# Kernel optimization log

Measured on AMD Instinct MI355X. Metric: run time of the kernel, lower is better.

Reference implementation:

```python
import jax, jax.numpy as jnp
import numpy as np

B, D, L = 32768, 1024, 4

def setup_inputs() -> dict:
    key = jax.random.key(0)
    k1, k2, k3 = jax.random.split(key, 3)
    x = jax.random.normal(k1, (B, D), dtype=jnp.float32)
    # torch init: normal_(0, 0.005) for both weights and biases, shape (d,1) -> flatten to (d,)
    weights = jax.random.normal(k2, (L, D), dtype=jnp.float32) * 0.005
    biases = jax.random.normal(k3, (L, D), dtype=jnp.float32) * 0.005
    return {"x": x, "weights": weights, "biases": biases}

def reference(x, weights, biases):
    # DCN cross layer: x_{i+1} = x0 * (x_i . w_i) + b_i + x_i
    # Algebraically identical to matmul(bmm(x0, x_i^T), w_i) + b_i + x_i
    x0 = x  # [B, D]

    def step(cur, wb):
        w, b = wb  # [D], [D]
        s = cur @ w  # [B] scalar per row (x_i^T w_i)
        cur = x0 * s[:, None] + b[None, :] + cur  # [B, D]
        return cur, None

    out, _ = jax.lax.scan(step, x, (weights, biases))
    return out  # [B, D] (squeeze of [B, D, 1])
```

## Files before the change

### kernel.cpp

```cpp
#include <hip/hip_runtime.h>


#define DCN_D 1024
#define DCN_F4 (DCN_D / 4)


__global__ __launch_bounds__(256) void dcn_pre_kernel(
    const float* __restrict__ w,
    const float* __restrict__ b,
    float* __restrict__ ws)
{
    const int t = threadIdx.x;
    for (int d = t; d < DCN_D; d += 256)
        ws[d] = b[d] + b[DCN_D + d] + b[2 * DCN_D + d] + b[3 * DCN_D + d];
    float p[6] = {0, 0, 0, 0, 0, 0};
    for (int d = t; d < DCN_D; d += 256) {
        const float b0 = b[d], b1 = b[DCN_D + d], b2 = b[2 * DCN_D + d];
        const float w1 = w[DCN_D + d], w2 = w[2 * DCN_D + d], w3 = w[3 * DCN_D + d];
        p[0] = fmaf(b0, w1, p[0]);
        p[1] = fmaf(b0, w2, p[1]);
        p[2] = fmaf(b1, w2, p[2]);
        p[3] = fmaf(b0, w3, p[3]);
        p[4] = fmaf(b1, w3, p[4]);
        p[5] = fmaf(b2, w3, p[5]);
    }
    __shared__ float red[6][4];
    const int wave = t >> 6, lane = t & 63;
    #pragma unroll
    for (int k = 0; k < 6; ++k) {
        float v = p[k];
        #pragma unroll
        for (int off = 32; off > 0; off >>= 1) v += __shfl_down(v, off, 64);
        if (lane == 0) red[k][wave] = v;
    }
    __syncthreads();
    if (t < 6) ws[DCN_D + t] = red[t][0] + red[t][1] + red[t][2] + red[t][3];
}

__device__ __forceinline__ float dot4acc(const float4 a, const float4 b, float acc) {
    return fmaf(a.x, b.x, fmaf(a.y, b.y, fmaf(a.z, b.z, fmaf(a.w, b.w, acc))));
}

__global__ __launch_bounds__(256) void dcn_main_kernel(
    const float* __restrict__ x,
    const float* __restrict__ w,
    const float* __restrict__ ws,
    float* __restrict__ out,
    int B)
{
    __shared__ float4 w_lds[4 * DCN_F4];
    __shared__ float4 b_lds[DCN_F4];

    const int t    = (int)threadIdx.x;
    const int lane = t & 63;
    const int wib  = t >> 6;
    const int row0 = ((int)blockIdx.x * 4 + wib) * 2;
    const bool live = row0 < B;
    const bool has2 = (row0 + 1) < B;

    float4 xa[4], xb[4];
    if (live) {
        const float4* __restrict__ xr0 =
            reinterpret_cast<const float4*>(x + (size_t)row0 * DCN_D);
        const float4* __restrict__ xr1 =
            reinterpret_cast<const float4*>(x + (size_t)(has2 ? row0 + 1 : row0) * DCN_D);
        #pragma unroll
        for (int j = 0; j < 4; ++j) xa[j] = xr0[lane + 64 * j];
        #pragma unroll
        for (int j = 0; j < 4; ++j) xb[j] = xr1[lane + 64 * j];
    }

    const float4* __restrict__ w4  = reinterpret_cast<const float4*>(w);
    const float4* __restrict__ bs4 = reinterpret_cast<const float4*>(ws);
    #pragma unroll
    for (int i = 0; i < 4; ++i) w_lds[t + 256 * i] = w4[t + 256 * i];
    b_lds[t] = bs4[t];
    const float c01   = ws[DCN_D + 0];
    const float c2sum = ws[DCN_D + 1] + ws[DCN_D + 2];
    const float c3sum = ws[DCN_D + 3] + ws[DCN_D + 4] + ws[DCN_D + 5];
    __syncthreads();

    if (!live) return;

    float p0[4] = {0, 0, 0, 0}, p1[4] = {0, 0, 0, 0};
    #pragma unroll
    for (int j = 0; j < 4; ++j) {
        const int idx = lane + 64 * j;
        #pragma unroll
        for (int l = 0; l < 4; ++l) {
            const float4 wv = w_lds[l * DCN_F4 + idx];
            p0[l] = dot4acc(xa[j], wv, p0[l]);
            p1[l] = dot4acc(xb[j], wv, p1[l]);
        }
    }

    #pragma unroll
    for (int off = 1; off < 64; off <<= 1) {
        #pragma unroll
        for (int l = 0; l < 4; ++l) {
            p0[l] += __shfl_xor(p0[l], off, 64);
            p1[l] += __shfl_xor(p1[l], off, 64);
        }
    }

    const float t1a = 1.f + p0[0];
    const float s1a = fmaf(p0[1], t1a, c01);
    const float t2a = t1a + s1a;
    const float s2a = fmaf(p0[2], t2a, c2sum);
    const float t3a = t2a + s2a;
    const float s3a = fmaf(p0[3], t3a, c3sum);
    const float S0  = t3a + s3a;
    const float t1b = 1.f + p1[0];
    const float s1b = fmaf(p1[1], t1b, c01);
    const float t2b = t1b + s1b;
    const float s2b = fmaf(p1[2], t2b, c2sum);
    const float t3b = t2b + s2b;
    const float s3b = fmaf(p1[3], t3b, c3sum);
    const float S1  = t3b + s3b;

    float4* __restrict__ o0 = reinterpret_cast<float4*>(out + (size_t)row0 * DCN_D);
    float4* __restrict__ o1 = reinterpret_cast<float4*>(out + (size_t)(row0 + 1) * DCN_D);
    #pragma unroll
    for (int j = 0; j < 4; ++j) {
        const int idx = lane + 64 * j;
        const float4 bb = b_lds[idx];
        float4 a;
        a.x = fmaf(xa[j].x, S0, bb.x);
        a.y = fmaf(xa[j].y, S0, bb.y);
        a.z = fmaf(xa[j].z, S0, bb.z);
        a.w = fmaf(xa[j].w, S0, bb.w);
        o0[idx] = a;
        if (has2) {
            float4 c;
            c.x = fmaf(xb[j].x, S1, bb.x);
            c.y = fmaf(xb[j].y, S1, bb.y);
            c.z = fmaf(xb[j].z, S1, bb.z);
            c.w = fmaf(xb[j].w, S1, bb.w);
            o1[idx] = c;
        }
    }
}

extern "C" void kernel_launch(void* const* d_in, const int* in_sizes, int n_in,
                              void* d_out, int out_size, void* d_ws, size_t ws_size,
                              hipStream_t stream) {
    const float* x = (const float*)d_in[0];
    const float* w = (const float*)d_in[1];
    const float* b = (const float*)d_in[2];
    float* out = (float*)d_out;
    float* ws = (float*)d_ws;
    const int B = in_sizes[0] / DCN_D;

    dcn_pre_kernel<<<1, 256, 0, stream>>>(w, b, ws);
    const int rows_per_block = 8;
    dcn_main_kernel<<<(B + rows_per_block - 1) / rows_per_block, 256, 0, stream>>>(
        x, w, ws, out, B);
}
```

Measured before the change: 50.43 us.

## Split fused DCN kernel into separate dot and update kernels

Breaks the single main kernel into a dots kernel that writes one scale per row to workspace and an update kernel that rereads x and writes the output. The fallback and dots paths also drop the shared-memory staging of weights and biases and read them straight from global/cache. This is meant to cut per-thread register pressure, but it reads x twice (an extra 128MB) and adds a kernel launch.

```diff
diff --git a/kernel.cpp b/kernel.cpp
--- a/kernel.cpp
+++ b/kernel.cpp
@@ -4,15 +4,18 @@
 #define DCN_D 1024
 #define DCN_F4 (DCN_D / 4)
 
+__device__ __forceinline__ float dot4acc(const float4 a, const float4 b, float acc) {
+    return fmaf(a.x, b.x, fmaf(a.y, b.y, fmaf(a.z, b.z, fmaf(a.w, b.w, acc))));
+}
 
 __global__ __launch_bounds__(256) void dcn_pre_kernel(
     const float* __restrict__ w,
     const float* __restrict__ b,
-    float* __restrict__ ws)
+    float* __restrict__ wc)
 {
     const int t = threadIdx.x;
     for (int d = t; d < DCN_D; d += 256)
-        ws[d] = b[d] + b[DCN_D + d] + b[2 * DCN_D + d] + b[3 * DCN_D + d];
+        wc[d] = b[d] + b[DCN_D + d] + b[2 * DCN_D + d] + b[3 * DCN_D + d];
     float p[6] = {0, 0, 0, 0, 0, 0};
     for (int d = t; d < DCN_D; d += 256) {
         const float b0 = b[d], b1 = b[DCN_D + d], b2 = b[2 * DCN_D + d];
@@ -34,53 +37,142 @@
         if (lane == 0) red[k][wave] = v;
     }
     __syncthreads();
-    if (t < 6) ws[DCN_D + t] = red[t][0] + red[t][1] + red[t][2] + red[t][3];
-}
-
-__device__ __forceinline__ float dot4acc(const float4 a, const float4 b, float acc) {
-    return fmaf(a.x, b.x, fmaf(a.y, b.y, fmaf(a.z, b.z, fmaf(a.w, b.w, acc))));
-}
-
-__global__ __launch_bounds__(256) void dcn_main_kernel(
+    if (t < 6) wc[DCN_D + t] = red[t][0] + red[t][1] + red[t][2] + red[t][3];
+}
+
+__global__ __launch_bounds__(256) void dcn_dots_kernel(
     const float* __restrict__ x,
     const float* __restrict__ w,
-    const float* __restrict__ ws,
+    const float* __restrict__ wc,
+    float* __restrict__ S,
+    int B)
+{
+    const int wid  = (int)((blockIdx.x * 256u + threadIdx.x) >> 6);
+    const int lane = (int)(threadIdx.x & 63);
+    const int row0 = wid * 2;
+    if (row0 >= B) return;
+
+    const float4* __restrict__ xr0 =
+        reinterpret_cast<const float4*>(x + (size_t)row0 * DCN_D);
+    const float4* __restrict__ xr1 =
+        reinterpret_cast<const float4*>(x + (size_t)(row0 + 1) * DCN_D);
+    const float4* __restrict__ w4 = reinterpret_cast<const float4*>(w);
+
+    float4 xa[4], xb[4];
+    #pragma unroll
+    for (int j = 0; j < 4; ++j) xa[j] = xr0[lane + 64 * j];
+    #pragma unroll
+    for (int j = 0; j < 4; ++j) xb[j] = xr1[lane + 64 * j];
+
+    float p0[4] = {0, 0, 0, 0}, p1[4] = {0, 0, 0, 0};
+    #pragma unroll
+    for (int j = 0; j < 4; ++j) {
+        const int idx = lane + 64 * j;
+        #pragma unroll
+        for (int l = 0; l < 4; ++l) {
+            const float4 wv = w4[l * DCN_F4 + idx];
+            p0[l] = dot4acc(xa[j], wv, p0[l]);
+            p1[l] = dot4acc(xb[j], wv, p1[l]);
+        }
+    }
+    #pragma unroll
+    for (int off = 1; off < 64; off <<= 1) {
+        #pragma unroll
+        for (int l = 0; l < 4; ++l) {
+            p0[l] += __shfl_xor(p0[l], off, 64);
+            p1[l] += __shfl_xor(p1[l], off, 64);
+        }
+    }
+
+    const float c01   = wc[DCN_D + 0];
+    const float c2sum = wc[DCN_D + 1] + wc[DCN_D + 2];
+    const float c3sum = wc[DCN_D + 3] + wc[DCN_D + 4] + wc[DCN_D + 5];
+
+    const float t1a = 1.f + p0[0];
+    const float s1a = fmaf(p0[1], t1a, c01);
+    const float t2a = t1a + s1a;
+    const float s2a = fmaf(p0[2], t2a, c2sum);
+    const float t3a = t2a + s2a;
+    const float s3a = fmaf(p0[3], t3a, c3sum);
+    const float t1b = 1.f + p1[0];
+    const float s1b = fmaf(p1[1], t1b, c01);
+    const float t2b = t1b + s1b;
+    const float s2b = fmaf(p1[2], t2b, c2sum);
+    const float t3b = t2b + s2b;
+    const float s3b = fmaf(p1[3], t3b, c3sum);
+
+    if (lane == 0) {
+        S[row0]     = t3a + s3a;
+        S[row0 + 1] = t3b + s3b;
+    }
+}
+
+__global__ __launch_bounds__(256) void dcn_update_kernel(
+    const float* __restrict__ x,
+    const float* __restrict__ S,
+    const float* __restrict__ wc,
     float* __restrict__ out,
     int B)
 {
-    __shared__ float4 w_lds[4 * DCN_F4];
-    __shared__ float4 b_lds[DCN_F4];
-
-    const int t    = (int)threadIdx.x;
-    const int lane = t & 63;
-    const int wib  = t >> 6;
-    const int row0 = ((int)blockIdx.x * 4 + wib) * 2;
-    const bool live = row0 < B;
-    const bool has2 = (row0 + 1) < B;
-
+    const int wid  = (int)((blockIdx.x * 256u + threadIdx.x) >> 6);
+    const int lane = (int)(threadIdx.x & 63);
+    const int row0 = wid * 2;
+    if (row0 >= B) return;
+
+    const float S0 = S[row0];
+    const float S1 = S[row0 + 1];
+
+    const float4* __restrict__ xr0 =
+        reinterpret_cast<const float4*>(x + (size_t)row0 * DCN_D);
+    const float4* __restrict__ xr1 =
+        reinterpret_cast<const float4*>(x + (size_t)(row0 + 1) * DCN_D);
+    const float4* __restrict__ bs4 = reinterpret_cast<const float4*>(wc);
+    float4* __restrict__ o0 = reinterpret_cast<float4*>(out + (size_t)row0 * DCN_D);
+    float4* __restrict__ o1 = reinterpret_cast<float4*>(out + (size_t)(row0 + 1) * DCN_D);
+
+    #pragma unroll
+    for (int j = 0; j < 4; ++j) {
+        const int idx = lane + 64 * j;
+        const float4 xa = xr0[idx];
+        const float4 xb = xr1[idx];
+        const float4 bb = bs4[idx];
+        float4 a;
+        a.x = fmaf(xa.x, S0, bb.x);
+        a.y = fmaf(xa.y, S0, bb.y);
+        a.z = fmaf(xa.z, S0, bb.z);
+        a.w = fmaf(xa.w, S0, bb.w);
+        o0[idx] = a;
+        float4 c;
+        c.x = fmaf(xb.x, S1, bb.x);
+        c.y = fmaf(xb.y, S1, bb.y);
+        c.z = fmaf(xb.z, S1, bb.z);
+        c.w = fmaf(xb.w, S1, bb.w);
+        o1[idx] = c;
+    }
+}
+
+__global__ __launch_bounds__(256) void dcn_main_fallback(
+    const float* __restrict__ x,
+    const float* __restrict__ w,
+    const float* __restrict__ wc,
+    float* __restrict__ out,
+    int B)
+{
+    const int wid  = (int)((blockIdx.x * 256u + threadIdx.x) >> 6);
+    const int lane = (int)(threadIdx.x & 63);
+    const int row0 = wid * 2;
+    if (row0 >= B) return;
+
+    const float4* __restrict__ xr0 =
+        reinterpret_cast<const float4*>(x + (size_t)row0 * DCN_D);
+    const float4* __restrict__ xr1 =
+        reinterpret_cast<const float4*>(x + (size_t)(row0 + 1) * DCN_D);
+    const float4* __restrict__ w4  = reinterpret_cast<const float4*>(w);
     float4 xa[4], xb[4];
-    if (live) {
-        const float4* __restrict__ xr0 =
-            reinterpret_cast<const float4*>(x + (size_t)row0 * DCN_D);
-        const float4* __restrict__ xr1 =
-            reinterpret_cast<const float4*>(x + (size_t)(has2 ? row0 + 1 : row0) * DCN_D);
-        #pragma unroll
-        for (int j = 0; j < 4; ++j) xa[j] = xr0[lane + 64 * j];
-        #pragma unroll
-        for (int j = 0; j < 4; ++j) xb[j] = xr1[lane + 64 * j];
-    }
-
-    const float4* __restrict__ w4  = reinterpret_cast<const float4*>(w);
-    const float4* __restrict__ bs4 = reinterpret_cast<const float4*>(ws);
-    #pragma unroll
-    for (int i = 0; i < 4; ++i) w_lds[t + 256 * i] = w4[t + 256 * i];
-    b_lds[t] = bs4[t];
-    const float c01   = ws[DCN_D + 0];
-    const float c2sum = ws[DCN_D + 1] + ws[DCN_D + 2];
-    const float c3sum = ws[DCN_D + 3] + ws[DCN_D + 4] + ws[DCN_D + 5];
-    __syncthreads();
-
-    if (!live) return;
+    #pragma unroll
+    for (int j = 0; j < 4; ++j) xa[j] = xr0[lane + 64 * j];
+    #pragma unroll
+    for (int j = 0; j < 4; ++j) xb[j] = xr1[lane + 64 * j];
 
     float p0[4] = {0, 0, 0, 0}, p1[4] = {0, 0, 0, 0};
     #pragma unroll
@@ -88,12 +180,11 @@
         const int idx = lane + 64 * j;
         #pragma unroll
         for (int l = 0; l < 4; ++l) {
-            const float4 wv = w_lds[l * DCN_F4 + idx];
+            const float4 wv = w4[l * DCN_F4 + idx];
             p0[l] = dot4acc(xa[j], wv, p0[l]);
             p1[l] = dot4acc(xb[j], wv, p1[l]);
         }
     }
-
     #pragma unroll
     for (int off = 1; off < 64; off <<= 1) {
         #pragma unroll
@@ -102,7 +193,9 @@
             p1[l] += __shfl_xor(p1[l], off, 64);
         }
     }
-
+    const float c01   = wc[DCN_D + 0];
+    const float c2sum = wc[DCN_D + 1] + wc[DCN_D + 2];
+    const float c3sum = wc[DCN_D + 3] + wc[DCN_D + 4] + wc[DCN_D + 5];
     const float t1a = 1.f + p0[0];
     const float s1a = fmaf(p0[1], t1a, c01);
     const float t2a = t1a + s1a;
@@ -118,26 +211,25 @@
     const float s3b = fmaf(p1[3], t3b, c3sum);
     const float S1  = t3b + s3b;
 
+    const float4* __restrict__ bs4 = reinterpret_cast<const float4*>(wc);
     float4* __restrict__ o0 = reinterpret_cast<float4*>(out + (size_t)row0 * DCN_D);
     float4* __restrict__ o1 = reinterpret_cast<float4*>(out + (size_t)(row0 + 1) * DCN_D);
     #pragma unroll
     for (int j = 0; j < 4; ++j) {
         const int idx = lane + 64 * j;
-        const float4 bb = b_lds[idx];
+        const float4 bb = bs4[idx];
         float4 a;
         a.x = fmaf(xa[j].x, S0, bb.x);
         a.y = fmaf(xa[j].y, S0, bb.y);
         a.z = fmaf(xa[j].z, S0, bb.z);
         a.w = fmaf(xa[j].w, S0, bb.w);
         o0[idx] = a;
-        if (has2) {
-            float4 c;
-            c.x = fmaf(xb[j].x, S1, bb.x);
-            c.y = fmaf(xb[j].y, S1, bb.y);
-            c.z = fmaf(xb[j].z, S1, bb.z);
-            c.w = fmaf(xb[j].w, S1, bb.w);
-            o1[idx] = c;
-        }
+        float4 c;
+        c.x = fmaf(xb[j].x, S1, bb.x);
+        c.y = fmaf(xb[j].y, S1, bb.y);
+        c.z = fmaf(xb[j].z, S1, bb.z);
+        c.w = fmaf(xb[j].w, S1, bb.w);
+        o1[idx] = c;
     }
 }
 
@@ -151,8 +243,19 @@
     float* ws = (float*)d_ws;
     const int B = in_sizes[0] / DCN_D;
 
-    dcn_pre_kernel<<<1, 256, 0, stream>>>(w, b, ws);
+    const size_t need = ((size_t)B + DCN_D + 16) * sizeof(float);
     const int rows_per_block = 8;
-    dcn_main_kernel<<<(B + rows_per_block - 1) / rows_per_block, 256, 0, stream>>>(
-        x, w, ws, out, B);
-}
+    const int grid = (B + rows_per_block - 1) / rows_per_block;
+
+    if (ws_size >= need) {
+        float* S  = ws;
+        float* wc = ws + B;
+        dcn_pre_kernel<<<1, 256, 0, stream>>>(w, b, wc);
+        dcn_dots_kernel<<<grid, 256, 0, stream>>>(x, w, wc, S, B);
+        dcn_update_kernel<<<grid, 256, 0, stream>>>(x, S, wc, out, B);
+    } else {
+        float* wc = ws;
+        dcn_pre_kernel<<<1, 256, 0, stream>>>(w, b, wc);
+        dcn_main_fallback<<<grid, 256, 0, stream>>>(x, w, wc, out, B);
+    }
+}
```

Result: slower. 71.17 us (+41.1%).
